# Kernel optimization log

Hardware: AMD Instinct MI355X
Metric: run time of the kernel (lower is better)

Reference implementation:

```python
import jax, jax.numpy as jnp
import numpy as np

B, T, D_IN = 2048, 26, 512
H = 512          # hidden_size
E = 256          # num_char_embeddings
C = 97           # num_class
S = 32           # num_steps = batch_max_length + 1


def setup_inputs() -> dict:
    key = jax.random.key(0)
    ks = jax.random.split(key, 16)
    sc = lambda n: 1.0 / np.sqrt(n)
    inp = {
        "batch_H": jax.random.normal(ks[0], (B, T, D_IN), jnp.float32),
        "text": jax.random.randint(ks[1], (B, S), 0, C),
        # attention cell params
        "W_i2h": jax.random.normal(ks[2], (H, D_IN), jnp.float32) * sc(D_IN),
        "W_h2h": jax.random.normal(ks[3], (H, H), jnp.float32) * sc(H),
        "b_h2h": jax.random.normal(ks[4], (H,), jnp.float32) * sc(H),
        "w_score": jax.random.normal(ks[5], (1, H), jnp.float32) * sc(H),
        # LSTMCell params (gate order: i, f, g, o)
        "W_ih": jax.random.normal(ks[6], (4 * H, D_IN + E), jnp.float32) * sc(D_IN + E),
        "W_hh": jax.random.normal(ks[7], (4 * H, H), jnp.float32) * sc(H),
        "b_ih": jax.random.normal(ks[8], (4 * H,), jnp.float32) * sc(H),
        "b_hh": jax.random.normal(ks[9], (4 * H,), jnp.float32) * sc(H),
        # generator + char embedding
        "W_gen": jax.random.normal(ks[10], (C, H), jnp.float32) * sc(H),
        "b_gen": jax.random.normal(ks[11], (C,), jnp.float32) * sc(H),
        "emb_table": jax.random.normal(ks[12], (C, E), jnp.float32),
    }
    return inp


def _decode(batch_H, text, W_i2h, W_h2h, b_h2h, w_score,
            W_ih, W_hh, b_ih, b_hh, emb_table):
    # i2h(batch_H) is constant across steps -> hoist out of the loop
    Hp = jnp.einsum('btd,hd->bth', batch_H, W_i2h)          # [B,T,H]
    char_embs = emb_table[text]                              # [B,S,E]
    h0 = jnp.zeros((batch_H.shape[0], H), batch_H.dtype)
    c0 = jnp.zeros_like(h0)

    def step(carry, ce):
        h, c = carry
        ph = h @ W_h2h.T + b_h2h                             # [B,H]
        e = jnp.tanh(Hp + ph[:, None, :]) @ w_score[0]       # [B,T]
        alpha = jax.nn.softmax(e, axis=1)                    # [B,T]
        context = jnp.einsum('bt,btd->bd', alpha, batch_H)   # [B,D_IN]
        x = jnp.concatenate([context, ce], axis=1)           # [B,D_IN+E]
        gates = x @ W_ih.T + b_ih + h @ W_hh.T + b_hh        # [B,4H]
        i, f, g, o = jnp.split(gates, 4, axis=1)
        c_new = jax.nn.sigmoid(f) * c + jax.nn.sigmoid(i) * jnp.tanh(g)
        h_new = jax.nn.sigmoid(o) * jnp.tanh(c_new)
        return (h_new, c_new), h_new

    _, hs = jax.lax.scan(step, (h0, c0), jnp.swapaxes(char_embs, 0, 1))
    return jnp.swapaxes(hs, 0, 1)                            # [B,S,H]


def reference(batch_H, text, W_i2h, W_h2h, b_h2h, w_score,
              W_ih, W_hh, b_ih, b_hh, W_gen, b_gen, emb_table):
    output_hiddens = _decode(batch_H, text, W_i2h, W_h2h, b_h2h, w_score,
                             W_ih, W_hh, b_ih, b_hh, emb_table)
    probs = output_hiddens @ W_gen.T + b_gen                 # [B,S,C]
    return probs
```

## Files before the change

### kernel.cpp

```cpp
#include <hip/hip_runtime.h>

#define BB 2048
#define TT 26
#define DIN 512
#define HH 512
#define EE 256
#define CC 97
#define SS 32
#define G4 2048
#define XK2 1024

typedef unsigned short u16;
typedef __bf16 bf16x8 __attribute__((ext_vector_type(8)));
typedef float f32x4 __attribute__((ext_vector_type(4)));

__device__ __forceinline__ float bf2f(u16 u) {
    return __uint_as_float(((unsigned int)u) << 16);
}
__device__ __forceinline__ u16 f2bf(float f) {
    unsigned int u = __float_as_uint(f);
    u = u + 0x7FFFu + ((u >> 16) & 1u);
    return (u16)(u >> 16);
}
__device__ __forceinline__ float th_f(float x) {
    return 1.0f - 2.0f * __builtin_amdgcn_rcpf(__expf(2.0f * x) + 1.0f);
}
__device__ __forceinline__ float sig_f(float x) {
    return __builtin_amdgcn_rcpf(1.0f + __expf(-x));
}

__device__ __forceinline__ void async16(const u16* g, u16* l) {
    __builtin_amdgcn_global_load_lds(
        (const __attribute__((address_space(1))) unsigned int*)(g),
        (__attribute__((address_space(3))) unsigned int*)(l), 16, 0, 0);
}

__global__ __launch_bounds__(256) void gemm128(
    const u16* __restrict__ A, int lda,
    const u16* __restrict__ W,
    u16* __restrict__ Cout, int ldc, int K)
{
    __shared__ __align__(16) u16 As[2 * 128 * 32];
    __shared__ __align__(16) u16 Ws[2 * 128 * 32];

    const int tid  = threadIdx.x;
    const int lane = tid & 63;
    const int wave = tid >> 6;

    int b = blockIdx.y * 4 + blockIdx.x;
    int swz = (b & 7) * 208 + (b >> 3);
    const int m0 = (swz >> 2) * 128;
    const int n0 = (swz & 3) * 128;

    const int srow = tid >> 2;
    const int scol = (tid & 3) * 8;
    const u16* Arow0 = A + (size_t)(m0 + srow) * lda + scol;
    const u16* Arow1 = A + (size_t)(m0 + 64 + srow) * lda + scol;
    const u16* Wrow0 = W + (size_t)(n0 + srow) * K + scol;
    const u16* Wrow1 = W + (size_t)(n0 + 64 + srow) * K + scol;

    const int wm = (wave >> 1) * 64;
    const int wn = (wave & 1) * 64;
    const int fr = lane & 15;
    const int fq = lane >> 4;

    f32x4 acc[4][4];
    #pragma unroll
    for (int i = 0; i < 4; i++)
        #pragma unroll
        for (int j = 0; j < 4; j++)
            #pragma unroll
            for (int r = 0; r < 4; r++) acc[i][j][r] = 0.0f;

    for (int kb = 0; kb < K; kb += 64) {
        #pragma unroll
        for (int cc = 0; cc < 2; cc++) {
            int k0 = kb + cc * 32;
            async16(Arow0 + k0, As + cc * 4096 + wave * 512);
            async16(Arow1 + k0, As + cc * 4096 + 2048 + wave * 512);
            async16(Wrow0 + k0, Ws + cc * 4096 + wave * 512);
            async16(Wrow1 + k0, Ws + cc * 4096 + 2048 + wave * 512);
        }
        __syncthreads();
        #pragma unroll
        for (int cc = 0; cc < 2; cc++) {
            const u16* A_ = As + cc * 4096;
            const u16* W_ = Ws + cc * 4096;
            bf16x8 af[4], bw[4];
            #pragma unroll
            for (int i = 0; i < 4; i++)
                af[i] = *(const bf16x8*)&A_[(wm + i * 16 + fr) * 32 + fq * 8];
            #pragma unroll
            for (int j = 0; j < 4; j++)
                bw[j] = *(const bf16x8*)&W_[(wn + j * 16 + fr) * 32 + fq * 8];
            #pragma unroll
            for (int i = 0; i < 4; i++)
                #pragma unroll
                for (int j = 0; j < 4; j++)
                    acc[i][j] = __builtin_amdgcn_mfma_f32_16x16x32_bf16(
                        af[i], bw[j], acc[i][j], 0, 0, 0);
        }
        __syncthreads();
    }

    #pragma unroll
    for (int j = 0; j < 4; j++) {
        int col = n0 + wn + j * 16 + fr;
        #pragma unroll
        for (int i = 0; i < 4; i++) {
            int row = m0 + wm + i * 16 + fq * 4;
            #pragma unroll
            for (int r = 0; r < 4; r++)
                Cout[(size_t)(row + r) * ldc + col] = f2bf(acc[i][j][r]);
        }
    }
}

__global__ __launch_bounds__(256) void gen128(
    const u16* __restrict__ A,
    const u16* __restrict__ Wg,
    const float* __restrict__ bgen,
    float* __restrict__ out)
{
    __shared__ __align__(16) u16 As[2 * 128 * 32];
    __shared__ __align__(16) u16 Ws[2 * 128 * 32];

    const int tid  = threadIdx.x;
    const int lane = tid & 63;
    const int wave = tid >> 6;
    const int m0 = blockIdx.y * 128;

    const int srow = tid >> 2;
    const int scol = (tid & 3) * 8;
    const u16* Arow0 = A + (size_t)(m0 + srow) * HH + scol;
    const u16* Arow1 = A + (size_t)(m0 + 64 + srow) * HH + scol;
    const u16* Wrow0 = Wg + (size_t)srow * HH + scol;
    const u16* Wrow1 = Wg + (size_t)(64 + srow) * HH + scol;

    const int wm = (wave >> 1) * 64;
    const int wn = (wave & 1) * 64;
    const int fr = lane & 15;
    const int fq = lane >> 4;

    f32x4 acc[4][4];
    #pragma unroll
    for (int i = 0; i < 4; i++)
        #pragma unroll
        for (int j = 0; j < 4; j++)
            #pragma unroll
            for (int r = 0; r < 4; r++) acc[i][j][r] = 0.0f;

    #pragma unroll
    for (int kb = 0; kb < HH; kb += 64) {
        #pragma unroll
        for (int cc = 0; cc < 2; cc++) {
            int k0 = kb + cc * 32;
            async16(Arow0 + k0, As + cc * 4096 + wave * 512);
            async16(Arow1 + k0, As + cc * 4096 + 2048 + wave * 512);
            async16(Wrow0 + k0, Ws + cc * 4096 + wave * 512);
            async16(Wrow1 + k0, Ws + cc * 4096 + 2048 + wave * 512);
        }
        __syncthreads();
        #pragma unroll
        for (int cc = 0; cc < 2; cc++) {
            const u16* A_ = As + cc * 4096;
            const u16* W_ = Ws + cc * 4096;
            bf16x8 af[4], bw[4];
            #pragma unroll
            for (int i = 0; i < 4; i++)
                af[i] = *(const bf16x8*)&A_[(wm + i * 16 + fr) * 32 + fq * 8];
            #pragma unroll
            for (int j = 0; j < 4; j++)
                bw[j] = *(const bf16x8*)&W_[(wn + j * 16 + fr) * 32 + fq * 8];
            #pragma unroll
            for (int i = 0; i < 4; i++)
                #pragma unroll
                for (int j = 0; j < 4; j++)
                    acc[i][j] = __builtin_amdgcn_mfma_f32_16x16x32_bf16(
                        af[i], bw[j], acc[i][j], 0, 0, 0);
        }
        __syncthreads();
    }

    #pragma unroll
    for (int j = 0; j < 4; j++) {
        int col = wn + j * 16 + fr;
        if (col < CC) {
            float bv = bgen[col];
            #pragma unroll
            for (int i = 0; i < 4; i++) {
                int row = m0 + wm + i * 16 + fq * 4;
                #pragma unroll
                for (int r = 0; r < 4; r++) {
                    int m = row + r;
                    int s = m >> 11, b = m & (BB - 1);
                    out[(size_t)b * (SS * CC) + s * CC + col] = acc[i][j][r] + bv;
                }
            }
        }
    }
}

__global__ __launch_bounds__(256) void gates_lstm(
    const u16* __restrict__ ctx,
    const u16* __restrict__ hprev,
    const u16* __restrict__ Wc,
    const float* __restrict__ bcat,
    const float* __restrict__ P,
    const int* __restrict__ text,
    float* __restrict__ c,
    u16* __restrict__ hnext,
    int s)
{
    __shared__ __align__(16) char smem[49152];
    __shared__ int text_sm[64];

    u16* As = (u16*)smem;
    u16* Ws = (u16*)(smem + 16384);

    const int tid  = threadIdx.x;
    const int lane = tid & 63;
    const int wave = tid >> 6;

    int b   = blockIdx.y * gridDim.x + blockIdx.x;
    int xcd = b & 7, loc = b >> 3;
    int by = (xcd & 3) * 8 + (loc & 7);
    int bx = (xcd >> 2) * 8 + (loc >> 3);
    const int m0 = by * 64;
    const int n0 = bx * 128;

    if (tid < 64) text_sm[tid] = text[(m0 + tid) * SS + s];

    const int srow = tid >> 2;
    const int scol = (tid & 3) * 8;
    const u16* Actx  = ctx   + (size_t)(m0 + srow) * 512 + scol;
    const u16* Ahid  = hprev + (size_t)(m0 + srow) * 512 + scol;
    const u16* Wrow0 = Wc + (size_t)(n0 + srow) * XK2 + scol;
    const u16* Wrow1 = Wc + (size_t)(n0 + 64 + srow) * XK2 + scol;

    const int wm = (wave & 1) * 32;
    const int wn = (wave >> 1) * 64;
    const int fr = lane & 15;
    const int fq = lane >> 4;

    f32x4 acc[2][4];
    #pragma unroll
    for (int i = 0; i < 2; i++)
        #pragma unroll
        for (int j = 0; j < 4; j++)
            #pragma unroll
            for (int r = 0; r < 4; r++) acc[i][j][r] = 0.0f;

    #pragma unroll
    for (int it = 0; it < 8; it++) {
        int kb = it * 128;
        #pragma unroll
        for (int cc = 0; cc < 4; cc++) {
            int k0 = kb + cc * 32;
            const u16* a = (k0 < 512) ? (Actx + k0) : (Ahid + (k0 - 512));
            async16(a, As + cc * 2048 + wave * 512);
            async16(Wrow0 + k0, Ws + cc * 4096 + wave * 512);
            async16(Wrow1 + k0, Ws + cc * 4096 + 2048 + wave * 512);
        }
        __syncthreads();
        #pragma unroll
        for (int cc = 0; cc < 4; cc++) {
            const u16* A_ = As + cc * 2048;
            const u16* W_ = Ws + cc * 4096;
            bf16x8 af[2], bw[4];
            #pragma unroll
            for (int i = 0; i < 2; i++)
                af[i] = *(const bf16x8*)&A_[(wm + i * 16 + fr) * 32 + fq * 8];
            #pragma unroll
            for (int j = 0; j < 4; j++)
                bw[j] = *(const bf16x8*)&W_[(wn + j * 16 + fr) * 32 + fq * 8];
            #pragma unroll
            for (int i = 0; i < 2; i++)
                #pragma unroll
                for (int j = 0; j < 4; j++)
                    acc[i][j] = __builtin_amdgcn_mfma_f32_16x16x32_bf16(
                        af[i], bw[j], acc[i][j], 0, 0, 0);
        }
        __syncthreads();
    }

    float* gsm = (float*)smem;
    #pragma unroll
    for (int p = 0; p < 2; p++) {
        if ((wave >> 1) == p) {
            #pragma unroll
            for (int j = 0; j < 4; j++) {
                int cl = j * 16 + fr;
                #pragma unroll
                for (int i = 0; i < 2; i++) {
                    int rl = wm + i * 16 + fq * 4;
                    #pragma unroll
                    for (int r = 0; r < 4; r++)
                        gsm[(rl + r) * 68 + cl] = acc[i][j][r];
                }
            }
        }
        __syncthreads();
        #pragma unroll
        for (int rr = 0; rr < 4; rr++) {
            int idx = rr * 256 + tid;
            int u = idx & 15, row = idx >> 4;
            int base = row * 68 + 4 * u;
            int hg = (n0 >> 2) + p * 16 + u;
            int c0 = 4 * hg;
            int ch = text_sm[row];
            float4 bc = *(const float4*)(bcat + c0);
            float4 pv = *(const float4*)(P + (size_t)ch * G4 + c0);
            float ig = sig_f(gsm[base]     + bc.x + pv.x);
            float fg = sig_f(gsm[base + 1] + bc.y + pv.y);
            float gg = th_f (gsm[base + 2] + bc.z + pv.z);
            float og = sig_f(gsm[base + 3] + bc.w + pv.w);
            size_t ci = (size_t)(m0 + row) * HH + hg;
            float cn = fg * c[ci] + ig * gg;
            c[ci] = cn;
            hnext[(size_t)(m0 + row) * HH + hg] = f2bf(og * th_f(cn));
        }
        __syncthreads();
    }
}

__global__ __launch_bounds__(256) void ph64(
    const u16* __restrict__ A,
    const u16* __restrict__ W,
    const float* __restrict__ bias,
    float* __restrict__ out)
{
    __shared__ __align__(16) u16 As[4 * 64 * 32];
    __shared__ __align__(16) u16 Ws[4 * 64 * 32];

    const int tid  = threadIdx.x;
    const int lane = tid & 63;
    const int wave = tid >> 6;

    int b   = blockIdx.x;
    int swz = (b & 7) * 32 + (b >> 3);
    const int m0 = (swz >> 3) * 64;
    const int n0 = (swz & 7) * 64;

    const int srow = tid >> 2;
    const int scol = (tid & 3) * 8;
    const u16* Arow = A + (size_t)(m0 + srow) * HH + scol;
    const u16* Wrow = W + (size_t)(n0 + srow) * HH + scol;

    const int wm = (wave >> 1) * 32;
    const int wn = (wave & 1) * 32;
    const int fr = lane & 15;
    const int fq = lane >> 4;

    f32x4 acc[2][2];
    #pragma unroll
    for (int i = 0; i < 2; i++)
        #pragma unroll
        for (int j = 0; j < 2; j++)
            #pragma unroll
            for (int r = 0; r < 4; r++) acc[i][j][r] = 0.0f;

    #pragma unroll
    for (int it = 0; it < 4; it++) {
        int kb = it * 128;
        #pragma unroll
        for (int cc = 0; cc < 4; cc++) {
            int k0 = kb + cc * 32;
            async16(Arow + k0, As + cc * 2048 + wave * 512);
            async16(Wrow + k0, Ws + cc * 2048 + wave * 512);
        }
        __syncthreads();
        #pragma unroll
        for (int cc = 0; cc < 4; cc++) {
            const u16* A_ = As + cc * 2048;
            const u16* W_ = Ws + cc * 2048;
            bf16x8 af[2], bw[2];
            #pragma unroll
            for (int mm = 0; mm < 2; mm++)
                af[mm] = *(const bf16x8*)&A_[(wm + mm * 16 + fr) * 32 + fq * 8];
            #pragma unroll
            for (int nn = 0; nn < 2; nn++)
                bw[nn] = *(const bf16x8*)&W_[(wn + nn * 16 + fr) * 32 + fq * 8];
            #pragma unroll
            for (int mm = 0; mm < 2; mm++)
                #pragma unroll
                for (int nn = 0; nn < 2; nn++)
                    acc[mm][nn] = __builtin_amdgcn_mfma_f32_16x16x32_bf16(
                        af[mm], bw[nn], acc[mm][nn], 0, 0, 0);
        }
        __syncthreads();
    }

    #pragma unroll
    for (int nn = 0; nn < 2; nn++) {
        int col = n0 + wn + nn * 16 + fr;
        float bv = bias[col];
        #pragma unroll
        for (int mm = 0; mm < 2; mm++) {
            int row = m0 + wm + mm * 16 + fq * 4;
            #pragma unroll
            for (int r = 0; r < 4; r++)
                out[(size_t)(row + r) * HH + col] = acc[mm][nn][r] + bv;
        }
    }
}

__global__ __launch_bounds__(256) void gemm64(
    const u16* __restrict__ A, int lda,
    const u16* __restrict__ W, int ldw,
    const float* __restrict__ bias,
    float* __restrict__ Cout, int ldc, int K, int use_bias)
{
    __shared__ __align__(16) u16 As[64][32];
    __shared__ __align__(16) u16 Ws[64][32];

    const int tid  = threadIdx.x;
    const int lane = tid & 63;
    const int wave = tid >> 6;
    const int m0 = blockIdx.y * 64;
    const int n0 = blockIdx.x * 64;
    const int ar = tid >> 2;
    const int ac = (tid & 3) * 8;
    const int wm = (wave >> 1) * 32;
    const int wn = (wave & 1) * 32;
    const int fr = lane & 15;
    const int fq = lane >> 4;

    f32x4 acc[2][2];
    #pragma unroll
    for (int i = 0; i < 2; i++)
        #pragma unroll
        for (int j = 0; j < 2; j++)
            #pragma unroll
            for (int r = 0; r < 4; r++) acc[i][j][r] = 0.0f;

    const u16* Arow = A + (size_t)(m0 + ar) * lda;
    const u16* Wrow = W + (size_t)(n0 + ar) * ldw;

    for (int k0 = 0; k0 < K; k0 += 32) {
        *(uint4*)&As[ar][ac] = *(const uint4*)(Arow + k0 + ac);
        *(uint4*)&Ws[ar][ac] = *(const uint4*)(Wrow + k0 + ac);
        __syncthreads();
        bf16x8 af[2], bw[2];
        #pragma unroll
        for (int mm = 0; mm < 2; mm++)
            af[mm] = *(const bf16x8*)&As[wm + mm * 16 + fr][fq * 8];
        #pragma unroll
        for (int nn = 0; nn < 2; nn++)
            bw[nn] = *(const bf16x8*)&Ws[wn + nn * 16 + fr][fq * 8];
        #pragma unroll
        for (int mm = 0; mm < 2; mm++)
            #pragma unroll
            for (int nn = 0; nn < 2; nn++)
                acc[mm][nn] = __builtin_amdgcn_mfma_f32_16x16x32_bf16(
                    af[mm], bw[nn], acc[mm][nn], 0, 0, 0);
        __syncthreads();
    }

    #pragma unroll
    for (int nn = 0; nn < 2; nn++) {
        int col = n0 + wn + nn * 16 + fr;
        float bv = use_bias ? bias[col] : 0.0f;
        #pragma unroll
        for (int mm = 0; mm < 2; mm++) {
            int row = m0 + wm + mm * 16 + fq * 4;
            #pragma unroll
            for (int r = 0; r < 4; r++)
                Cout[(size_t)(row + r) * ldc + col] = acc[mm][nn][r] + bv;
        }
    }
}

__global__ __launch_bounds__(256) void attn_step(
    const u16* __restrict__ Hp, const float* __restrict__ ph,
    const float* __restrict__ wscore, const u16* __restrict__ bH16,
    u16* __restrict__ ctx)
{
    const int b = blockIdx.x;
    const int tid = threadIdx.x, lane = tid & 63, wave = tid >> 6;
    __shared__ float e_sm[32];
    __shared__ float alpha_sm[32];

    const int h8 = lane * 8;
    float ph_r[8], ws_r[8];
    {
        float4 p0 = *(const float4*)(ph + (size_t)b * HH + h8);
        float4 p1 = *(const float4*)(ph + (size_t)b * HH + h8 + 4);
        ph_r[0]=p0.x; ph_r[1]=p0.y; ph_r[2]=p0.z; ph_r[3]=p0.w;
        ph_r[4]=p1.x; ph_r[5]=p1.y; ph_r[6]=p1.z; ph_r[7]=p1.w;
        float4 w0 = *(const float4*)(wscore + h8);
        float4 w1 = *(const float4*)(wscore + h8 + 4);
        ws_r[0]=w0.x; ws_r[1]=w0.y; ws_r[2]=w0.z; ws_r[3]=w0.w;
        ws_r[4]=w1.x; ws_r[5]=w1.y; ws_r[6]=w1.z; ws_r[7]=w1.w;
    }

    for (int t = wave; t < TT; t += 4) {
        uint4 hv = *(const uint4*)(Hp + ((size_t)b * TT + t) * HH + h8);
        const u16* hu = (const u16*)&hv;
        float sum = 0.0f;
        #pragma unroll
        for (int j = 0; j < 8; j++)
            sum += th_f(bf2f(hu[j]) + ph_r[j]) * ws_r[j];
        #pragma unroll
        for (int off = 32; off > 0; off >>= 1) sum += __shfl_down(sum, off);
        if (lane == 0) e_sm[t] = sum;
    }
    __syncthreads();

    if (wave == 0) {
        float ev = (lane < TT) ? e_sm[lane] : -3.0e38f;
        float mx = ev;
        #pragma unroll
        for (int off = 32; off > 0; off >>= 1)
            mx = fmaxf(mx, __shfl_xor(mx, off));
        float p = (lane < TT) ? __expf(ev - mx) : 0.0f;
        float ssum = p;
        #pragma unroll
        for (int off = 32; off > 0; off >>= 1) ssum += __shfl_xor(ssum, off);
        if (lane < TT) alpha_sm[lane] = p / ssum;
    }
    __syncthreads();

    {
        int d0 = tid * 2;
        float c0 = 0.0f, c1 = 0.0f;
        const u16* bb = bH16 + (size_t)b * TT * DIN + d0;
        #pragma unroll
        for (int t = 0; t < TT; t++) {
            unsigned int v = *(const unsigned int*)(bb + (size_t)t * DIN);
            float a = alpha_sm[t];
            c0 += a * bf2f((u16)(v & 0xffffu));
            c1 += a * bf2f((u16)(v >> 16));
        }
        unsigned int o = (unsigned int)f2bf(c0) | ((unsigned int)f2bf(c1) << 16);
        *(unsigned int*)(ctx + (size_t)b * 512 + d0) = o;
    }
}

__global__ __launch_bounds__(256) void cast_f32_bf16(
    const float* __restrict__ src, u16* __restrict__ dst, int n)
{
    int i = (blockIdx.x * 256 + threadIdx.x) * 4;
    if (i < n) {
        float4 v = *(const float4*)(src + i);
        ushort4 o;
        o.x = f2bf(v.x); o.y = f2bf(v.y); o.z = f2bf(v.z); o.w = f2bf(v.w);
        *(ushort4*)(dst + i) = o;
    }
}

__global__ __launch_bounds__(256) void prep_all(
    const float* __restrict__ W_ih, const float* __restrict__ W_hh,
    const float* __restrict__ b_ih, const float* __restrict__ b_hh,
    const float* __restrict__ b_h2h, const float* __restrict__ emb,
    const float* __restrict__ W_i2h, const float* __restrict__ W_h2h,
    const float* __restrict__ W_gen,
    u16* __restrict__ Wcat, u16* __restrict__ Wce16, u16* __restrict__ emb16,
    u16* __restrict__ Wgen16, u16* __restrict__ Wi2h16, u16* __restrict__ Wh2h16,
    float* __restrict__ bcat, float* __restrict__ cst, u16* __restrict__ hid0,
    float* __restrict__ ph)
{
    int i = blockIdx.x * 256 + threadIdx.x;

    {
        int np = i >> 10, k = i & (XK2 - 1);
        int h = np >> 2, g = np & 3;
        int n = g * HH + h;
        float v = (k < 512) ? W_ih[(size_t)n * (DIN + EE) + k]
                            : W_hh[(size_t)n * HH + (k - 512)];
        Wcat[(size_t)i] = f2bf(v);
    }
    if (i < G4 * EE) {
        int np = i >> 8, e = i & (EE - 1);
        int h = np >> 2, g = np & 3;
        int n = g * HH + h;
        Wce16[i] = f2bf(W_ih[(size_t)n * (DIN + EE) + DIN + e]);
    }
    if (i < 128 * EE) {
        int ch = i >> 8, e = i & (EE - 1);
        emb16[i] = (ch < CC) ? f2bf(emb[(size_t)ch * EE + e]) : (u16)0;
    }
    if (i < 128 * HH) {
        int n = i >> 9, k = i & (HH - 1);
        Wgen16[i] = (n < CC) ? f2bf(W_gen[(size_t)n * HH + k]) : (u16)0;
    }
    if (i < HH * DIN) Wi2h16[i] = f2bf(W_i2h[i]);
    if (i < HH * HH)  Wh2h16[i] = f2bf(W_h2h[i]);
    if (i < G4) {
        int h = i >> 2, g = i & 3;
        int n = g * HH + h;
        bcat[i] = b_ih[n] + b_hh[n];
    }
    if (i < BB * HH) {
        cst[i] = 0.0f;
        hid0[i] = 0;
        ph[i] = b_h2h[i & (HH - 1)];
    }
}

#define BH16_OFF  ((size_t)0)
#define HP_OFF    ((size_t)54525952)
#define HID_OFF   ((size_t)109051904)
#define CTX_OFF   ((size_t)178257920)
#define WCAT_OFF  ((size_t)180355072)
#define WCE_OFF   ((size_t)184549376)
#define EMB16_OFF ((size_t)185597952)
#define WGEN_OFF  ((size_t)185663488)
#define WI2H_OFF  ((size_t)185794560)
#define WH2H_OFF  ((size_t)186318848)
#define BCAT_OFF  ((size_t)186843136)
#define P_OFF     ((size_t)186851328)
#define PH_OFF    ((size_t)187899904)
#define CST_OFF   ((size_t)192094208)

extern "C" void kernel_launch(void* const* d_in, const int* in_sizes, int n_in,
                              void* d_out, int out_size, void* d_ws, size_t ws_size,
                              hipStream_t stream)
{
    const float* batch_H = (const float*)d_in[0];
    const int*   text    = (const int*)d_in[1];
    const float* W_i2h   = (const float*)d_in[2];
    const float* W_h2h   = (const float*)d_in[3];
    const float* b_h2h   = (const float*)d_in[4];
    const float* w_score = (const float*)d_in[5];
    const float* W_ih    = (const float*)d_in[6];
    const float* W_hh    = (const float*)d_in[7];
    const float* b_ih    = (const float*)d_in[8];
    const float* b_hh    = (const float*)d_in[9];
    const float* W_gen   = (const float*)d_in[10];
    const float* b_gen   = (const float*)d_in[11];
    const float* emb     = (const float*)d_in[12];

    char* ws = (char*)d_ws;
    u16*   bH16   = (u16*)(ws + BH16_OFF);
    u16*   Hp     = (u16*)(ws + HP_OFF);
    u16*   hid    = (u16*)(ws + HID_OFF);
    u16*   ctx    = (u16*)(ws + CTX_OFF);
    u16*   Wcat   = (u16*)(ws + WCAT_OFF);
    u16*   Wce16  = (u16*)(ws + WCE_OFF);
    u16*   emb16  = (u16*)(ws + EMB16_OFF);
    u16*   Wgen16 = (u16*)(ws + WGEN_OFF);
    u16*   Wi2h16 = (u16*)(ws + WI2H_OFF);
    u16*   Wh2h16 = (u16*)(ws + WH2H_OFF);
    float* bcat   = (float*)(ws + BCAT_OFF);
    float* P      = (float*)(ws + P_OFF);
    float* ph     = (float*)(ws + PH_OFF);
    float* cst    = (float*)(ws + CST_OFF);
    float* out    = (float*)d_out;

    cast_f32_bf16<<<dim3((BB * TT * DIN / 4 + 255) / 256), 256, 0, stream>>>(
        batch_H, bH16, BB * TT * DIN);
    prep_all<<<dim3((G4 * XK2) / 256), 256, 0, stream>>>(
        W_ih, W_hh, b_ih, b_hh, b_h2h, emb, W_i2h, W_h2h, W_gen,
        Wcat, Wce16, emb16, Wgen16, Wi2h16, Wh2h16, bcat, cst, hid, ph);
    gemm64<<<dim3(G4 / 64, 128 / 64), 256, 0, stream>>>(
        emb16, EE, Wce16, EE, nullptr, P, G4, EE, 0);

    gemm128<<<dim3(HH / 128, (BB * TT) / 128), 256, 0, stream>>>(
        bH16, DIN, Wi2h16, Hp, HH, DIN);

    for (int s = 0; s < SS; s++) {
        u16* hprev = hid + (size_t)s * BB * HH;
        u16* hnext = hid + (size_t)(s + 1) * BB * HH;

        attn_step<<<dim3(BB), 256, 0, stream>>>(Hp, ph, w_score, bH16, ctx);

        gates_lstm<<<dim3(G4 / 128, BB / 64), 256, 0, stream>>>(
            ctx, hprev, Wcat, bcat, P, text, cst, hnext, s);

        ph64<<<dim3(256), 256, 0, stream>>>(hnext, Wh2h16, b_h2h, ph);
    }

    gen128<<<dim3(1, (SS * BB) / 128), 256, 0, stream>>>(
        hid + (size_t)BB * HH, Wgen16, b_gen, out);
}
```

Before: 1.584 ms.

## Fuse h2h projection into LSTM gates kernel via per-row-block atomic barrier

Removes the separate ph64 launch each step. Each gates_lstm block now increments a per-row-block counter, spins until all 16 column blocks of its 64-row slab have written hnext, then computes a 64x32 slice of h@W_h2h^T+b into ph. This cuts 32 kernel launches and their gaps. The cost is a spin-wait barrier that assumes all 16 co-dependent blocks are resident at once (512 blocks total), which risks stalls or a bounded-spin timeout that would give wrong results.

```diff
diff --git a/kernel.cpp b/kernel.cpp
--- a/kernel.cpp
+++ b/kernel.cpp
@@ -210,7 +210,11 @@
     const int* __restrict__ text,
     float* __restrict__ c,
     u16* __restrict__ hnext,
-    int s)
+    int s,
+    const u16* __restrict__ Wh2h,
+    const float* __restrict__ bh2h,
+    float* __restrict__ phout,
+    unsigned int* cnt)
 {
     __shared__ __align__(16) char smem[49152];
     __shared__ int text_sm[64];
@@ -322,85 +326,70 @@
         }
         __syncthreads();
     }
-}
-
-__global__ __launch_bounds__(256) void ph64(
-    const u16* __restrict__ A,
-    const u16* __restrict__ W,
-    const float* __restrict__ bias,
-    float* __restrict__ out)
-{
-    __shared__ __align__(16) u16 As[4 * 64 * 32];
-    __shared__ __align__(16) u16 Ws[4 * 64 * 32];
-
-    const int tid  = threadIdx.x;
-    const int lane = tid & 63;
-    const int wave = tid >> 6;
-
-    int b   = blockIdx.x;
-    int swz = (b & 7) * 32 + (b >> 3);
-    const int m0 = (swz >> 3) * 64;
-    const int n0 = (swz & 7) * 64;
-
-    const int srow = tid >> 2;
-    const int scol = (tid & 3) * 8;
-    const u16* Arow = A + (size_t)(m0 + srow) * HH + scol;
-    const u16* Wrow = W + (size_t)(n0 + srow) * HH + scol;
-
-    const int wm = (wave >> 1) * 32;
-    const int wn = (wave & 1) * 32;
-    const int fr = lane & 15;
-    const int fq = lane >> 4;
-
-    f32x4 acc[2][2];
-    #pragma unroll
-    for (int i = 0; i < 2; i++)
+
+    if (s != SS - 1) {
+        if (tid == 0) {
+            __threadfence();
+            __hip_atomic_fetch_add(&cnt[s * 32 + by], 1u,
+                                   __ATOMIC_RELEASE, __HIP_MEMORY_SCOPE_AGENT);
+            int spin = 0;
+            while (__hip_atomic_load(&cnt[s * 32 + by], __ATOMIC_ACQUIRE,
+                                     __HIP_MEMORY_SCOPE_AGENT) < 16u &&
+                   spin < (1 << 22)) {
+                __builtin_amdgcn_s_sleep(4);
+                ++spin;
+            }
+        }
+        __syncthreads();
+        __threadfence();
+
+        const int nc0 = bx * 32;
+        u16* Aps = (u16*)smem;
+        u16* Wps = (u16*)(smem + 16384);
+        const u16* Hrow  = hnext + (size_t)(m0 + srow) * 512 + scol;
+        const u16* Wprow = Wh2h + (size_t)(nc0 + ((tid & 127) >> 2)) * 512 + scol;
+        const int wm2 = wave * 16;
+
+        f32x4 pacc[2];
         #pragma unroll
         for (int j = 0; j < 2; j++)
             #pragma unroll
-            for (int r = 0; r < 4; r++) acc[i][j][r] = 0.0f;
-
-    #pragma unroll
-    for (int it = 0; it < 4; it++) {
-        int kb = it * 128;
-        #pragma unroll
-        for (int cc = 0; cc < 4; cc++) {
-            int k0 = kb + cc * 32;
-            async16(Arow + k0, As + cc * 2048 + wave * 512);
-            async16(Wrow + k0, Ws + cc * 2048 + wave * 512);
-        }
-        __syncthreads();
-        #pragma unroll
-        for (int cc = 0; cc < 4; cc++) {
-            const u16* A_ = As + cc * 2048;
-            const u16* W_ = Ws + cc * 2048;
-            bf16x8 af[2], bw[2];
-            #pragma unroll
-            for (int mm = 0; mm < 2; mm++)
-                af[mm] = *(const bf16x8*)&A_[(wm + mm * 16 + fr) * 32 + fq * 8];
-            #pragma unroll
-            for (int nn = 0; nn < 2; nn++)
-                bw[nn] = *(const bf16x8*)&W_[(wn + nn * 16 + fr) * 32 + fq * 8];
-            #pragma unroll
-            for (int mm = 0; mm < 2; mm++)
+            for (int r = 0; r < 4; r++) pacc[j][r] = 0.0f;
+
+        #pragma unroll
+        for (int win = 0; win < 4; win++) {
+            int kb = win * 128;
+            #pragma unroll
+            for (int cc2 = 0; cc2 < 4; cc2++) {
+                int k0 = kb + cc2 * 32;
+                async16(Hrow + k0, Aps + cc2 * 2048 + wave * 512);
+                if (wave < 2)
+                    async16(Wprow + k0, Wps + cc2 * 1024 + wave * 512);
+            }
+            __syncthreads();
+            #pragma unroll
+            for (int cc2 = 0; cc2 < 4; cc2++) {
+                bf16x8 af = *(const bf16x8*)
+                    &Aps[cc2 * 2048 + (wm2 + fr) * 32 + fq * 8];
                 #pragma unroll
-                for (int nn = 0; nn < 2; nn++)
-                    acc[mm][nn] = __builtin_amdgcn_mfma_f32_16x16x32_bf16(
-                        af[mm], bw[nn], acc[mm][nn], 0, 0, 0);
-        }
-        __syncthreads();
-    }
-
-    #pragma unroll
-    for (int nn = 0; nn < 2; nn++) {
-        int col = n0 + wn + nn * 16 + fr;
-        float bv = bias[col];
-        #pragma unroll
-        for (int mm = 0; mm < 2; mm++) {
-            int row = m0 + wm + mm * 16 + fq * 4;
+                for (int j = 0; j < 2; j++) {
+                    bf16x8 bw = *(const bf16x8*)
+                        &Wps[cc2 * 1024 + (j * 16 + fr) * 32 + fq * 8];
+                    pacc[j] = __builtin_amdgcn_mfma_f32_16x16x32_bf16(
+                        af, bw, pacc[j], 0, 0, 0);
+                }
+            }
+            __syncthreads();
+        }
+
+        #pragma unroll
+        for (int j = 0; j < 2; j++) {
+            int col = nc0 + j * 16 + fr;
+            float bv = bh2h[col];
+            int row = m0 + wm2 + fq * 4;
             #pragma unroll
             for (int r = 0; r < 4; r++)
-                out[(size_t)(row + r) * HH + col] = acc[mm][nn][r] + bv;
+                phout[(size_t)(row + r) * 512 + col] = pacc[j][r] + bv;
         }
     }
 }
@@ -558,7 +547,7 @@
     u16* __restrict__ Wcat, u16* __restrict__ Wce16, u16* __restrict__ emb16,
     u16* __restrict__ Wgen16, u16* __restrict__ Wi2h16, u16* __restrict__ Wh2h16,
     float* __restrict__ bcat, float* __restrict__ cst, u16* __restrict__ hid0,
-    float* __restrict__ ph)
+    float* __restrict__ ph, unsigned int* __restrict__ cnt)
 {
     int i = blockIdx.x * 256 + threadIdx.x;
 
@@ -596,6 +585,7 @@
         hid0[i] = 0;
         ph[i] = b_h2h[i & (HH - 1)];
     }
+    if (i < SS * 32) cnt[i] = 0u;
 }
 
 #define BH16_OFF  ((size_t)0)
@@ -612,6 +602,7 @@
 #define P_OFF     ((size_t)186851328)
 #define PH_OFF    ((size_t)187899904)
 #define CST_OFF   ((size_t)192094208)
+#define CNT_OFF   ((size_t)196288512)
 
 extern "C" void kernel_launch(void* const* d_in, const int* in_sizes, int n_in,
                               void* d_out, int out_size, void* d_ws, size_t ws_size,
@@ -646,13 +637,14 @@
     float* P      = (float*)(ws + P_OFF);
     float* ph     = (float*)(ws + PH_OFF);
     float* cst    = (float*)(ws + CST_OFF);
+    unsigned int* cnt = (unsigned int*)(ws + CNT_OFF);
     float* out    = (float*)d_out;
 
     cast_f32_bf16<<<dim3((BB * TT * DIN / 4 + 255) / 256), 256, 0, stream>>>(
         batch_H, bH16, BB * TT * DIN);
     prep_all<<<dim3((G4 * XK2) / 256), 256, 0, stream>>>(
         W_ih, W_hh, b_ih, b_hh, b_h2h, emb, W_i2h, W_h2h, W_gen,
-        Wcat, Wce16, emb16, Wgen16, Wi2h16, Wh2h16, bcat, cst, hid, ph);
+        Wcat, Wce16, emb16, Wgen16, Wi2h16, Wh2h16, bcat, cst, hid, ph, cnt);
     gemm64<<<dim3(G4 / 64, 128 / 64), 256, 0, stream>>>(
         emb16, EE, Wce16, EE, nullptr, P, G4, EE, 0);
 
@@ -666,9 +658,8 @@
         attn_step<<<dim3(BB), 256, 0, stream>>>(Hp, ph, w_score, bH16, ctx);
 
         gates_lstm<<<dim3(G4 / 128, BB / 64), 256, 0, stream>>>(
-            ctx, hprev, Wcat, bcat, P, text, cst, hnext, s);
-
-        ph64<<<dim3(256), 256, 0, stream>>>(hnext, Wh2h16, b_h2h, ph);
+            ctx, hprev, Wcat, bcat, P, text, cst, hnext, s,
+            Wh2h16, b_h2h, ph, cnt);
     }
 
     gen128<<<dim3(1, (SS * BB) / 128), 256, 0, stream>>>(
```

Result: slower. 4.187 ms (+164.3%).
